# Performance work log

Measured on AMD Instinct MI355X. Metric: run time of the kernel, lower is better.

Reference implementation:

```python
import jax, jax.numpy as jnp
import numpy as np

DIM = 768
HEADS = 12
EXPERTS = 8
HID = 3072  # dim * moe_mlp_ratio(=4)
TOP_K = 2
LN_EPS = 1e-5


def _layer_norm(x, g, b):
    mu = x.mean(-1, keepdims=True)
    var = ((x - mu) ** 2).mean(-1, keepdims=True)
    return (x - mu) * jax.lax.rsqrt(var + LN_EPS) * g + b


def setup_inputs() -> dict:
    key = jax.random.key(0)
    ks = jax.random.split(key, 16)
    s = 0.02
    return {
        "x": jax.random.normal(ks[0], (8, 196, DIM), jnp.float32),
        "ln1_g": jnp.ones((DIM,), jnp.float32),
        "ln1_b": jnp.zeros((DIM,), jnp.float32),
        "qkv_w": jax.random.normal(ks[1], (DIM, 3 * DIM), jnp.float32) * s,
        "qkv_b": jnp.zeros((3 * DIM,), jnp.float32),
        "proj_w": jax.random.normal(ks[2], (DIM, DIM), jnp.float32) * s,
        "proj_b": jnp.zeros((DIM,), jnp.float32),
        "ln2_g": jnp.ones((DIM,), jnp.float32),
        "ln2_b": jnp.zeros((DIM,), jnp.float32),
        "gate_w": jax.random.normal(ks[3], (DIM, EXPERTS), jnp.float32) * s,
        "w1": jax.random.normal(ks[4], (EXPERTS, DIM, HID), jnp.float32) * s,
        "b1": jnp.zeros((EXPERTS, HID), jnp.float32),
        "w2": jax.random.normal(ks[5], (EXPERTS, HID, DIM), jnp.float32) * s,
        "b2": jnp.zeros((EXPERTS, DIM), jnp.float32),
    }


def _attention(x, qkv_w, qkv_b, proj_w, proj_b):
    B, N, C = x.shape
    hd = C // HEADS
    qkv = (x @ qkv_w + qkv_b).reshape(B, N, 3, HEADS, hd).transpose(2, 0, 3, 1, 4)
    q, k, v = qkv[0], qkv[1], qkv[2]  # [B,H,N,hd]
    attn = jax.nn.softmax(jnp.einsum("bhnd,bhmd->bhnm", q, k) * (hd ** -0.5), axis=-1)
    o = jnp.einsum("bhnm,bhmd->bhnd", attn, v).transpose(0, 2, 1, 3).reshape(B, N, C)
    return o @ proj_w + proj_b


def _moe_mlp(xn, gate_w, w1, b1, w2, b2):
    # xn: [T, D]; noisy top-k gate in eval mode (no noise)
    T = xn.shape[0]
    logits = xn @ gate_w                                   # [T, E]
    top_logits, top_idx = jax.lax.top_k(logits, TOP_K)     # [T, k]
    top_gates = jax.nn.softmax(top_logits, axis=-1)        # [T, k]
    gates = jnp.zeros((T, EXPERTS), xn.dtype).at[
        jnp.arange(T)[:, None], top_idx
    ].set(top_gates)                                       # [T, E] sparse combine weights
    # dense-masked expert compute (math identical to dispatch: gate=0 tokens contribute 0)
    h = jax.nn.gelu(jnp.einsum("td,edh->teh", xn, w1) + b1, approximate=False)
    y = jnp.einsum("teh,ehd->ted", h, w2) + b2             # [T, E, D]
    return jnp.einsum("ted,te->td", y, gates)


def reference(x, ln1_g, ln1_b, qkv_w, qkv_b, proj_w, proj_b,
              ln2_g, ln2_b, gate_w, w1, b1, w2, b2):
    B, N, C = x.shape
    x = x + _attention(_layer_norm(x, ln1_g, ln1_b), qkv_w, qkv_b, proj_w, proj_b)
    xn = _layer_norm(x, ln2_g, ln2_b).reshape(B * N, C)
    moe_out = _moe_mlp(xn, gate_w, w1, b1, w2, b2).reshape(B, N, C)
    return x + moe_out
```

## Files before the change

kernel.cpp:

```cpp
#include <hip/hip_runtime.h>
#include <hip/hip_bf16.h>
#include <math.h>

#define DIMC 768
#define HEADS 12
#define HD 64
#define EXPERTS 8
#define HID 3072
#define BB 8
#define NN 196
#define TT (BB*NN)
#define CAP_ROWS 4224
#define LN_EPS 1e-5f

typedef float f32x4_t __attribute__((ext_vector_type(4)));
typedef short bf16x8_t __attribute__((ext_vector_type(8)));
typedef unsigned short u16x8_t __attribute__((ext_vector_type(8)));

__device__ __forceinline__ unsigned short f2bf(float f) {
    unsigned int u = __float_as_uint(f);
    u += 0x7FFFu + ((u >> 16) & 1u);
    return (unsigned short)(u >> 16);
}
__device__ __forceinline__ float bf2f(unsigned short u) {
    return __uint_as_float(((unsigned int)u) << 16);
}

__global__ void ln_kernel(const float* __restrict__ x, const float* __restrict__ g,
                          const float* __restrict__ b, float* __restrict__ out_f,
                          unsigned short* __restrict__ out_hi,
                          unsigned short* __restrict__ out_lo) {
    int t = blockIdx.x;
    const float* xr = x + (size_t)t * DIMC;
    int tid = threadIdx.x;
    float v0 = xr[tid], v1 = xr[tid + 256], v2 = xr[tid + 512];
    __shared__ float red[256];
    red[tid] = v0 + v1 + v2;
    __syncthreads();
    for (int off = 128; off > 0; off >>= 1) {
        if (tid < off) red[tid] += red[tid + off];
        __syncthreads();
    }
    float mu = red[0] * (1.0f / DIMC);
    __syncthreads();
    float d0 = v0 - mu, d1 = v1 - mu, d2 = v2 - mu;
    red[tid] = d0*d0 + d1*d1 + d2*d2;
    __syncthreads();
    for (int off = 128; off > 0; off >>= 1) {
        if (tid < off) red[tid] += red[tid + off];
        __syncthreads();
    }
    float rstd = rsqrtf(red[0] * (1.0f / DIMC) + LN_EPS);
    float o0 = d0 * rstd * g[tid]       + b[tid];
    float o1 = d1 * rstd * g[tid + 256] + b[tid + 256];
    float o2 = d2 * rstd * g[tid + 512] + b[tid + 512];
    if (out_f) {
        float* o = out_f + (size_t)t * DIMC;
        o[tid] = o0; o[tid + 256] = o1; o[tid + 512] = o2;
    }
    if (out_hi) {
        unsigned short* o = out_hi + (size_t)t * DIMC;
        unsigned short h0 = f2bf(o0), h1 = f2bf(o1), h2 = f2bf(o2);
        o[tid] = h0; o[tid + 256] = h1; o[tid + 512] = h2;
        if (out_lo) {
            unsigned short* ol = out_lo + (size_t)t * DIMC;
            ol[tid]       = f2bf(o0 - bf2f(h0));
            ol[tid + 256] = f2bf(o1 - bf2f(h1));
            ol[tid + 512] = f2bf(o2 - bf2f(h2));
        }
    }
}

__global__ void attn_mfma_kernel(const float* __restrict__ qkv,
                                 unsigned short* __restrict__ ao_h,
                                 unsigned short* __restrict__ ao_l) {
    __shared__ float ps[64][224];
    __shared__ unsigned short QsH[64 * 64], QsL[64 * 64];
    __shared__ unsigned short KsH[64 * 64], KsL[64 * 64];

    int bh = blockIdx.x;
    int b = bh / HEADS, h = bh % HEADS;
    int q0 = blockIdx.y * 64;
    const float* base = qkv + (size_t)b * NN * 2304 + h * 64;

    int tid = threadIdx.x;
    int sr = tid >> 3, sq = tid & 7;
    int lane = tid & 63;
    int wid = tid >> 6;
    int wm = (wid >> 1) * 32;
    int wn = (wid & 1) * 32;
    int lrow = lane & 15;
    int lq = lane >> 4;
    int colb_base = lq * 16;

    #pragma unroll
    for (int p = 0; p < 2; ++p) {
        int r = sr + p * 32;
        int n = q0 + r;
        float v[8] = {0.f,0.f,0.f,0.f,0.f,0.f,0.f,0.f};
        if (n < NN) {
            float4 a0 = *(const float4*)(base + (size_t)n * 2304 + sq * 8);
            float4 a1 = *(const float4*)(base + (size_t)n * 2304 + sq * 8 + 4);
            v[0]=a0.x; v[1]=a0.y; v[2]=a0.z; v[3]=a0.w;
            v[4]=a1.x; v[5]=a1.y; v[6]=a1.z; v[7]=a1.w;
        }
        u16x8_t hv, lv;
        #pragma unroll
        for (int t = 0; t < 8; ++t) {
            unsigned short hh = f2bf(v[t]);
            hv[t] = hh; lv[t] = f2bf(v[t] - bf2f(hh));
        }
        int off = r * 128 + ((sq * 16) ^ ((r & 7) << 4));
        *(u16x8_t*)((char*)QsH + off) = hv;
        *(u16x8_t*)((char*)QsL + off) = lv;
    }

    for (int kt = 0; kt < 4; ++kt) {
        int j0 = kt * 64;
        __syncthreads();
        #pragma unroll
        for (int p = 0; p < 2; ++p) {
            int r = sr + p * 32;
            int n = j0 + r;
            float v[8] = {0.f,0.f,0.f,0.f,0.f,0.f,0.f,0.f};
            if (n < NN) {
                float4 a0 = *(const float4*)(base + (size_t)n * 2304 + 768 + sq * 8);
                float4 a1 = *(const float4*)(base + (size_t)n * 2304 + 768 + sq * 8 + 4);
                v[0]=a0.x; v[1]=a0.y; v[2]=a0.z; v[3]=a0.w;
                v[4]=a1.x; v[5]=a1.y; v[6]=a1.z; v[7]=a1.w;
            }
            u16x8_t hv, lv;
            #pragma unroll
            for (int t = 0; t < 8; ++t) {
                unsigned short hh = f2bf(v[t]);
                hv[t] = hh; lv[t] = f2bf(v[t] - bf2f(hh));
            }
            int off = r * 128 + ((sq * 16) ^ ((r & 7) << 4));
            *(u16x8_t*)((char*)KsH + off) = hv;
            *(u16x8_t*)((char*)KsL + off) = lv;
        }
        __syncthreads();

        f32x4_t acc[2][2] = {};
        #pragma unroll
        for (int kk = 0; kk < 2; ++kk) {
            int colb = kk * 64 + colb_base;
            bf16x8_t qh[2], ql[2], kh[2], kl[2];
            #pragma unroll
            for (int i = 0; i < 2; ++i) {
                int ra = wm + i * 16 + lrow;
                int oa = ra * 128 + (colb ^ ((ra & 7) << 4));
                qh[i] = *(const bf16x8_t*)((const char*)QsH + oa);
                ql[i] = *(const bf16x8_t*)((const char*)QsL + oa);
                int rb = wn + i * 16 + lrow;
                int ob = rb * 128 + (colb ^ ((rb & 7) << 4));
                kh[i] = *(const bf16x8_t*)((const char*)KsH + ob);
                kl[i] = *(const bf16x8_t*)((const char*)KsL + ob);
            }
            #pragma unroll
            for (int mi = 0; mi < 2; ++mi)
                #pragma unroll
                for (int ni = 0; ni < 2; ++ni) {
                    acc[mi][ni] = __builtin_amdgcn_mfma_f32_16x16x32_bf16(
                        qh[mi], kh[ni], acc[mi][ni], 0, 0, 0);
                    acc[mi][ni] = __builtin_amdgcn_mfma_f32_16x16x32_bf16(
                        qh[mi], kl[ni], acc[mi][ni], 0, 0, 0);
                    acc[mi][ni] = __builtin_amdgcn_mfma_f32_16x16x32_bf16(
                        ql[mi], kh[ni], acc[mi][ni], 0, 0, 0);
                }
        }
        #pragma unroll
        for (int mi = 0; mi < 2; ++mi)
            #pragma unroll
            for (int ni = 0; ni < 2; ++ni) {
                int jc = j0 + wn + ni * 16 + lrow;
                if (jc < 224) {
                    int rowb = wm + mi * 16 + lq * 4;
                    #pragma unroll
                    for (int j = 0; j < 4; ++j)
                        ps[rowb + j][jc] = acc[mi][ni][j] * 0.125f;
                }
            }
    }
    __syncthreads();

    {
        int i = tid >> 2, l = tid & 3;
        float mx = -1e30f;
        for (int j = l; j < NN; j += 4) mx = fmaxf(mx, ps[i][j]);
        mx = fmaxf(mx, __shfl_xor(mx, 1, 4));
        mx = fmaxf(mx, __shfl_xor(mx, 2, 4));
        float sum = 0.f;
        for (int j = l; j < NN; j += 4) { float e = expf(ps[i][j] - mx); ps[i][j] = e; sum += e; }
        sum += __shfl_xor(sum, 1, 4);
        sum += __shfl_xor(sum, 2, 4);
        float inv = 1.f / sum;
        for (int j = l; j < NN; j += 4) ps[i][j] *= inv;
    }

    f32x4_t oacc[2][2] = {};
    for (int kt = 0; kt < 4; ++kt) {
        int j0 = kt * 64;
        __syncthreads();
        #pragma unroll
        for (int p = 0; p < 2; ++p) {
            int r = sr + p * 32;
            int n = j0 + r;
            float v[8] = {0.f,0.f,0.f,0.f,0.f,0.f,0.f,0.f};
            if (n < NN) {
                float4 a0 = *(const float4*)(base + (size_t)n * 2304 + 1536 + sq * 8);
                float4 a1 = *(const float4*)(base + (size_t)n * 2304 + 1536 + sq * 8 + 4);
                v[0]=a0.x; v[1]=a0.y; v[2]=a0.z; v[3]=a0.w;
                v[4]=a1.x; v[5]=a1.y; v[6]=a1.z; v[7]=a1.w;
            }
            #pragma unroll
            for (int t = 0; t < 8; ++t) {
                int d = sq * 8 + t;
                unsigned short hh = f2bf(v[t]);
                int off = d * 128 + ((r * 2) ^ ((d & 7) << 4));
                *(unsigned short*)((char*)KsH + off) = hh;
                *(unsigned short*)((char*)KsL + off) = f2bf(v[t] - bf2f(hh));
            }
        }
        __syncthreads();

        int kkmax = (kt == 3) ? 1 : 2;
        for (int kk = 0; kk < kkmax; ++kk) {
            int colb = kk * 64 + colb_base;
            bf16x8_t pah[2], pal[2], vh[2], vl[2];
            #pragma unroll
            for (int i = 0; i < 2; ++i) {
                int ra = wm + i * 16 + lrow;
                const float* prow = &ps[ra][j0 + kk * 32 + lq * 8];
                float4 a0 = *(const float4*)prow;
                float4 a1 = *(const float4*)(prow + 4);
                float vv[8] = {a0.x,a0.y,a0.z,a0.w,a1.x,a1.y,a1.z,a1.w};
                u16x8_t hv, lv;
                #pragma unroll
                for (int t = 0; t < 8; ++t) {
                    unsigned short hh = f2bf(vv[t]);
                    hv[t] = hh; lv[t] = f2bf(vv[t] - bf2f(hh));
                }
                pah[i] = *(bf16x8_t*)&hv;
                pal[i] = *(bf16x8_t*)&lv;
                int rb = wn + i * 16 + lrow;
                int ob = rb * 128 + (colb ^ ((rb & 7) << 4));
                vh[i] = *(const bf16x8_t*)((const char*)KsH + ob);
                vl[i] = *(const bf16x8_t*)((const char*)KsL + ob);
            }
            #pragma unroll
            for (int mi = 0; mi < 2; ++mi)
                #pragma unroll
                for (int ni = 0; ni < 2; ++ni) {
                    oacc[mi][ni] = __builtin_amdgcn_mfma_f32_16x16x32_bf16(
                        pah[mi], vh[ni], oacc[mi][ni], 0, 0, 0);
                    oacc[mi][ni] = __builtin_amdgcn_mfma_f32_16x16x32_bf16(
                        pah[mi], vl[ni], oacc[mi][ni], 0, 0, 0);
                    oacc[mi][ni] = __builtin_amdgcn_mfma_f32_16x16x32_bf16(
                        pal[mi], vh[ni], oacc[mi][ni], 0, 0, 0);
                }
        }
    }

    #pragma unroll
    for (int mi = 0; mi < 2; ++mi)
        #pragma unroll
        for (int ni = 0; ni < 2; ++ni) {
            int col = h * 64 + wn + ni * 16 + lrow;
            #pragma unroll
            for (int j = 0; j < 4; ++j) {
                int n = q0 + wm + mi * 16 + lq * 4 + j;
                if (n < NN) {
                    float v = oacc[mi][ni][j];
                    unsigned short hh = f2bf(v);
                    size_t o = (size_t)(b * NN + n) * DIMC + col;
                    ao_h[o] = hh;
                    ao_l[o] = f2bf(v - bf2f(hh));
                }
            }
        }
}

__global__ void gate_kernel(const float* __restrict__ xn, const float* __restrict__ gw,
                            int* __restrict__ tok_e, float* __restrict__ tok_g,
                            int* __restrict__ counts) {
    int t = blockIdx.x;
    int lane = threadIdx.x;
    float acc[8] = {};
    const float* xr = xn + (size_t)t * DIMC;
    for (int i = lane; i < DIMC; i += 64) {
        float xi = xr[i];
        const float* gr = gw + (size_t)i * 8;
        #pragma unroll
        for (int e = 0; e < 8; ++e) acc[e] += xi * gr[e];
    }
    #pragma unroll
    for (int e = 0; e < 8; ++e) {
        #pragma unroll
        for (int off = 32; off > 0; off >>= 1) acc[e] += __shfl_down(acc[e], off, 64);
    }
    if (lane == 0) {
        int e0 = 0; float l0 = acc[0];
        #pragma unroll
        for (int e = 1; e < 8; ++e) if (acc[e] > l0) { l0 = acc[e]; e0 = e; }
        int e1 = -1; float l1 = -3e38f;
        #pragma unroll
        for (int e = 0; e < 8; ++e) if (e != e0 && acc[e] > l1) { l1 = acc[e]; e1 = e; }
        float pp = expf(l1 - l0);
        float g0 = 1.f / (1.f + pp);
        float g1 = pp / (1.f + pp);
        tok_e[t*2] = e0; tok_e[t*2+1] = e1;
        tok_g[t*2] = g0; tok_g[t*2+1] = g1;
        atomicAdd(&counts[e0], 1);
        atomicAdd(&counts[e1], 1);
    }
}

__global__ void init_kernel(int* __restrict__ counts, int* __restrict__ row2tok, int cap) {
    int i = blockIdx.x * blockDim.x + threadIdx.x;
    if (i < 8) counts[i] = 0;
    if (i < cap) row2tok[i] = -1;
}

__global__ void offsets_kernel(const int* __restrict__ counts, int* __restrict__ offsets,
                               int* __restrict__ cursor) {
    if (threadIdx.x == 0 && blockIdx.x == 0) {
        int off = 0;
        for (int e = 0; e < 8; ++e) {
            offsets[e] = off;
            cursor[e]  = off;
            off += ((counts[e] + 63) / 64) * 64;
        }
        offsets[8] = off;
    }
}

__global__ void fill_kernel(const int* __restrict__ tok_e, int* __restrict__ cursor,
                            int* __restrict__ row2tok, int* __restrict__ tok_row) {
    int t = blockIdx.x * blockDim.x + threadIdx.x;
    if (t >= TT) return;
    #pragma unroll
    for (int k = 0; k < 2; ++k) {
        int e = tok_e[t*2+k];
        int slot = atomicAdd(&cursor[e], 1);
        row2tok[slot] = t;
        tok_row[t*2+k] = slot;
    }
}

__global__ void transpose_bf16(const float* __restrict__ src, unsigned short* __restrict__ dst,
                               int R, int C) {
    __shared__ float tile[64][65];
    const float* s = src + (size_t)blockIdx.z * R * C;
    unsigned short* d = dst + (size_t)blockIdx.z * R * C;
    int c0 = blockIdx.x * 64, r0 = blockIdx.y * 64;
    int tid = threadIdx.x;
    int tr = tid >> 4;
    int tc = (tid & 15) * 4;
    #pragma unroll
    for (int p = 0; p < 4; ++p) {
        int r = tr + p * 16;
        const float4 v = *(const float4*)(s + (size_t)(r0 + r) * C + c0 + tc);
        tile[r][tc+0] = v.x; tile[r][tc+1] = v.y; tile[r][tc+2] = v.z; tile[r][tc+3] = v.w;
    }
    __syncthreads();
    #pragma unroll
    for (int p = 0; p < 4; ++p) {
        int c = tr + p * 16;
        ushort4 o;
        o.x = f2bf(tile[tc+0][c]);
        o.y = f2bf(tile[tc+1][c]);
        o.z = f2bf(tile[tc+2][c]);
        o.w = f2bf(tile[tc+3][c]);
        *(ushort4*)(d + (size_t)(c0 + c) * R + r0 + tc) = o;
    }
}

__global__ void transpose_split_bf16(const float* __restrict__ src,
                                     unsigned short* __restrict__ dh,
                                     unsigned short* __restrict__ dl, int R, int C) {
    __shared__ float tile[64][65];
    int c0 = blockIdx.x * 64, r0 = blockIdx.y * 64;
    int tid = threadIdx.x;
    int tr = tid >> 4;
    int tc = (tid & 15) * 4;
    #pragma unroll
    for (int p = 0; p < 4; ++p) {
        int r = tr + p * 16;
        const float4 v = *(const float4*)(src + (size_t)(r0 + r) * C + c0 + tc);
        tile[r][tc+0] = v.x; tile[r][tc+1] = v.y; tile[r][tc+2] = v.z; tile[r][tc+3] = v.w;
    }
    __syncthreads();
    #pragma unroll
    for (int p = 0; p < 4; ++p) {
        int c = tr + p * 16;
        ushort4 h, l;
        float v0 = tile[tc+0][c], v1 = tile[tc+1][c], v2 = tile[tc+2][c], v3 = tile[tc+3][c];
        h.x = f2bf(v0); l.x = f2bf(v0 - bf2f(h.x));
        h.y = f2bf(v1); l.y = f2bf(v1 - bf2f(h.y));
        h.z = f2bf(v2); l.z = f2bf(v2 - bf2f(h.z));
        h.w = f2bf(v3); l.w = f2bf(v3 - bf2f(h.w));
        size_t off = (size_t)(c0 + c) * R + r0 + tc;
        *(ushort4*)(dh + off) = h;
        *(ushort4*)(dl + off) = l;
    }
}

template<int RES>
__global__ void mfma_gemm_split(const unsigned short* __restrict__ Ah,
                                const unsigned short* __restrict__ Al,
                                const unsigned short* __restrict__ Bth,
                                const unsigned short* __restrict__ Btl,
                                const float* __restrict__ bias,
                                const float* __restrict__ res,
                                float* __restrict__ C,
                                int M, int N, int K) {
    __shared__ unsigned short AsH[64 * 64];
    __shared__ unsigned short AsL[64 * 64];
    __shared__ unsigned short BsH[64 * 64];
    __shared__ unsigned short BsL[64 * 64];

    int m0 = blockIdx.x * 64;
    int n0 = blockIdx.y * 64;
    int tid = threadIdx.x;
    int sr = tid >> 3;
    int sq = tid & 7;
    int lane = tid & 63;
    int wid = tid >> 6;
    int wm = (wid >> 1) * 32;
    int wn = (wid & 1) * 32;
    int colb_base = (lane >> 4) * 16;
    int lrow = lane & 15;

    f32x4_t acc[2][2] = {};

    for (int k0 = 0; k0 < K; k0 += 64) {
        #pragma unroll
        for (int p = 0; p < 2; ++p) {
            int r = sr + p * 32;
            int swz = (sq * 16) ^ ((r & 7) << 4);
            int4 vah = {0,0,0,0}, val = {0,0,0,0};
            if (m0 + r < M) {
                size_t aoff = (size_t)(m0 + r) * K + k0 + sq * 8;
                vah = *(const int4*)(Ah + aoff);
                val = *(const int4*)(Al + aoff);
            }
            *(int4*)((char*)AsH + r * 128 + swz) = vah;
            *(int4*)((char*)AsL + r * 128 + swz) = val;
            size_t boff = (size_t)(n0 + r) * K + k0 + sq * 8;
            *(int4*)((char*)BsH + r * 128 + swz) = *(const int4*)(Bth + boff);
            *(int4*)((char*)BsL + r * 128 + swz) = *(const int4*)(Btl + boff);
        }
        __syncthreads();
        #pragma unroll
        for (int kk = 0; kk < 2; ++kk) {
            int colb = kk * 64 + colb_base;
            bf16x8_t ah[2], al[2], bh[2], bl[2];
            #pragma unroll
            for (int i = 0; i < 2; ++i) {
                int ra = wm + i * 16 + lrow;
                int oa = ra * 128 + (colb ^ ((ra & 7) << 4));
                ah[i] = *(const bf16x8_t*)((const char*)AsH + oa);
                al[i] = *(const bf16x8_t*)((const char*)AsL + oa);
                int rb = wn + i * 16 + lrow;
                int ob = rb * 128 + (colb ^ ((rb & 7) << 4));
                bh[i] = *(const bf16x8_t*)((const char*)BsH + ob);
                bl[i] = *(const bf16x8_t*)((const char*)BsL + ob);
            }
            #pragma unroll
            for (int mi = 0; mi < 2; ++mi)
                #pragma unroll
                for (int ni = 0; ni < 2; ++ni) {
                    acc[mi][ni] = __builtin_amdgcn_mfma_f32_16x16x32_bf16(
                        ah[mi], bh[ni], acc[mi][ni], 0, 0, 0);
                    acc[mi][ni] = __builtin_amdgcn_mfma_f32_16x16x32_bf16(
                        ah[mi], bl[ni], acc[mi][ni], 0, 0, 0);
                    acc[mi][ni] = __builtin_amdgcn_mfma_f32_16x16x32_bf16(
                        al[mi], bh[ni], acc[mi][ni], 0, 0, 0);
                }
        }
        __syncthreads();
    }

    #pragma unroll
    for (int mi = 0; mi < 2; ++mi) {
        #pragma unroll
        for (int ni = 0; ni < 2; ++ni) {
            int col = n0 + wn + ni * 16 + lrow;
            #pragma unroll
            for (int j = 0; j < 4; ++j) {
                int row = m0 + wm + mi * 16 + (lane >> 4) * 4 + j;
                if (row < M) {
                    float v = acc[mi][ni][j] + bias[col];
                    if (RES) v += res[(size_t)row * N + col];
                    C[(size_t)row * N + col] = v;
                }
            }
        }
    }
}

template<int GATHER, int GELU, int OUT_BF16>
__global__ void mfma_gemm_grouped(const unsigned short* __restrict__ A,
                                  const unsigned short* __restrict__ Bt,
                                  const float* __restrict__ bias,
                                  const int* __restrict__ offsets,
                                  const int* __restrict__ row2tok,
                                  void* __restrict__ Cout,
                                  int N, int K, int nxb) {
    __shared__ unsigned short As[64 * 64];
    __shared__ unsigned short Bs[64 * 64];
    __shared__ int toks[64];

    int nwg = gridDim.x;
    int pbid = blockIdx.x;
    int q = nwg >> 3, r8 = nwg & 7;
    int xcd = pbid & 7, slot = pbid >> 3;
    int L = (xcd < r8) ? xcd * (q + 1) + slot
                       : r8 * (q + 1) + (xcd - r8) * q + slot;
    int xb = L % nxb;
    int n0 = (L / nxb) * 64;
    int r0 = xb * 64;
    if (r0 >= offsets[8]) return;
    int e = 0;
    while (r0 >= offsets[e + 1]) ++e;

    int tid = threadIdx.x;
    if (GATHER && tid < 64) toks[tid] = row2tok[r0 + tid];
    __syncthreads();

    const unsigned short* Be = Bt + (size_t)e * N * K;

    int sr = tid >> 3;
    int sq = tid & 7;
    int lane = tid & 63;
    int wid = tid >> 6;
    int wm = (wid >> 1) * 32;
    int wn = (wid & 1) * 32;
    int colb_base = (lane >> 4) * 16;
    int lrow = lane & 15;

    f32x4_t acc[2][2] = {};

    for (int k0 = 0; k0 < K; k0 += 64) {
        #pragma unroll
        for (int p = 0; p < 2; ++p) {
            int r = sr + p * 32;
            int swz = (sq * 16) ^ ((r & 7) << 4);
            int4 va = {0, 0, 0, 0};
            if (GATHER) {
                int tok = toks[r];
                if (tok >= 0) va = *(const int4*)(A + (size_t)tok * K + k0 + sq * 8);
            } else {
                va = *(const int4*)(A + (size_t)(r0 + r) * K + k0 + sq * 8);
            }
            *(int4*)((char*)As + r * 128 + swz) = va;
            int4 vb = *(const int4*)(Be + (size_t)(n0 + r) * K + k0 + sq * 8);
            *(int4*)((char*)Bs + r * 128 + swz) = vb;
        }
        __syncthreads();
        #pragma unroll
        for (int kk = 0; kk < 2; ++kk) {
            int colb = kk * 64 + colb_base;
            bf16x8_t a[2], b[2];
            #pragma unroll
            for (int i = 0; i < 2; ++i) {
                int ra = wm + i * 16 + lrow;
                a[i] = *(const bf16x8_t*)((const char*)As + ra * 128 + (colb ^ ((ra & 7) << 4)));
                int rb = wn + i * 16 + lrow;
                b[i] = *(const bf16x8_t*)((const char*)Bs + rb * 128 + (colb ^ ((rb & 7) << 4)));
            }
            #pragma unroll
            for (int mi = 0; mi < 2; ++mi)
                #pragma unroll
                for (int ni = 0; ni < 2; ++ni)
                    acc[mi][ni] = __builtin_amdgcn_mfma_f32_16x16x32_bf16(
                        a[mi], b[ni], acc[mi][ni], 0, 0, 0);
        }
        __syncthreads();
    }

    #pragma unroll
    for (int mi = 0; mi < 2; ++mi) {
        #pragma unroll
        for (int ni = 0; ni < 2; ++ni) {
            int col = n0 + wn + ni * 16 + lrow;
            float bv = GELU ? bias[(size_t)e * N + col] : 0.f;
            #pragma unroll
            for (int j = 0; j < 4; ++j) {
                int row = r0 + wm + mi * 16 + (lane >> 4) * 4 + j;
                float v = acc[mi][ni][j] + bv;
                if (GELU) v = 0.5f * v * (1.f + erff(v * 0.70710678f));
                if (OUT_BF16)
                    ((unsigned short*)Cout)[(size_t)row * N + col] = f2bf(v);
                else
                    ((float*)Cout)[(size_t)row * N + col] = v;
            }
        }
    }
}

__global__ void combine_kernel(const float* __restrict__ x_res, const float* __restrict__ y,
                               const float* __restrict__ b2, const int* __restrict__ tok_e,
                               const float* __restrict__ tok_g, const int* __restrict__ tok_row,
                               float* __restrict__ out) {
    int t = blockIdx.x;
    int c = blockIdx.y * 256 + threadIdx.x;
    int e0 = tok_e[t*2], e1 = tok_e[t*2+1];
    float g0 = tok_g[t*2], g1 = tok_g[t*2+1];
    int r0 = tok_row[t*2], r1 = tok_row[t*2+1];
    float v = x_res[(size_t)t * DIMC + c]
            + g0 * (y[(size_t)r0 * DIMC + c] + b2[(size_t)e0 * DIMC + c])
            + g1 * (y[(size_t)r1 * DIMC + c] + b2[(size_t)e1 * DIMC + c]);
    out[(size_t)t * DIMC + c] = v;
}

extern "C" void kernel_launch(void* const* d_in, const int* in_sizes, int n_in,
                              void* d_out, int out_size, void* d_ws, size_t ws_size,
                              hipStream_t stream) {
    const float* x      = (const float*)d_in[0];
    const float* ln1_g  = (const float*)d_in[1];
    const float* ln1_b  = (const float*)d_in[2];
    const float* qkv_w  = (const float*)d_in[3];
    const float* qkv_b  = (const float*)d_in[4];
    const float* proj_w = (const float*)d_in[5];
    const float* proj_b = (const float*)d_in[6];
    const float* ln2_g  = (const float*)d_in[7];
    const float* ln2_b  = (const float*)d_in[8];
    const float* gate_w = (const float*)d_in[9];
    const float* w1     = (const float*)d_in[10];
    const float* b1     = (const float*)d_in[11];
    const float* w2     = (const float*)d_in[12];
    const float* b2     = (const float*)d_in[13];
    float* out = (float*)d_out;

    char* p = (char*)d_ws;
    auto alloc = [&](size_t nbytes) {
        void* r = (void*)p;
        p += (nbytes + 255) & ~(size_t)255;
        return r;
    };
    unsigned short* xn1_h   = (unsigned short*)alloc((size_t)TT * DIMC * 2);
    unsigned short* xn1_l   = (unsigned short*)alloc((size_t)TT * DIMC * 2);
    float*          qkv     = (float*)alloc((size_t)TT * 2304 * 4);
    unsigned short* ao_h    = (unsigned short*)alloc((size_t)TT * DIMC * 2);
    unsigned short* ao_l    = (unsigned short*)alloc((size_t)TT * DIMC * 2);
    float*          x_res   = (float*)alloc((size_t)TT * DIMC * 4);
    float*          xn2_f   = (float*)alloc((size_t)TT * DIMC * 4);
    unsigned short* xn2_bf  = (unsigned short*)alloc((size_t)TT * DIMC * 2);
    unsigned short* h       = (unsigned short*)alloc((size_t)CAP_ROWS * HID * 2);
    float*          y       = (float*)alloc((size_t)CAP_ROWS * DIMC * 4);
    unsigned short* w1t     = (unsigned short*)alloc((size_t)EXPERTS * DIMC * HID * 2);
    unsigned short* w2t     = (unsigned short*)alloc((size_t)EXPERTS * DIMC * HID * 2);
    unsigned short* qwt_h   = (unsigned short*)alloc((size_t)DIMC * 2304 * 2);
    unsigned short* qwt_l   = (unsigned short*)alloc((size_t)DIMC * 2304 * 2);
    unsigned short* pwt_h   = (unsigned short*)alloc((size_t)DIMC * DIMC * 2);
    unsigned short* pwt_l   = (unsigned short*)alloc((size_t)DIMC * DIMC * 2);
    float*          tok_g   = (float*)alloc((size_t)2 * TT * 4);
    int*            tok_e   = (int*)alloc((size_t)2 * TT * 4);
    int*            tok_row = (int*)alloc((size_t)2 * TT * 4);
    int*            row2tok = (int*)alloc((size_t)CAP_ROWS * 4);
    int*            counts  = (int*)alloc(32 * 4);
    int*            offsets = (int*)alloc(32 * 4);
    int*            cursor  = (int*)alloc(32 * 4);

    init_kernel<<<(CAP_ROWS + 255) / 256, 256, 0, stream>>>(counts, row2tok, CAP_ROWS);

    transpose_bf16<<<dim3(HID / 64, DIMC / 64, EXPERTS), 256, 0, stream>>>(w1, w1t, DIMC, HID);
    transpose_bf16<<<dim3(DIMC / 64, HID / 64, EXPERTS), 256, 0, stream>>>(w2, w2t, HID, DIMC);
    transpose_split_bf16<<<dim3(2304 / 64, DIMC / 64), 256, 0, stream>>>(qkv_w, qwt_h, qwt_l,
                                                                         DIMC, 2304);
    transpose_split_bf16<<<dim3(DIMC / 64, DIMC / 64), 256, 0, stream>>>(proj_w, pwt_h, pwt_l,
                                                                         DIMC, DIMC);

    ln_kernel<<<TT, 256, 0, stream>>>(x, ln1_g, ln1_b, nullptr, xn1_h, xn1_l);

    mfma_gemm_split<0><<<dim3((TT + 63) / 64, 2304 / 64), 256, 0, stream>>>(
        xn1_h, xn1_l, qwt_h, qwt_l, qkv_b, nullptr, qkv, TT, 2304, DIMC);

    attn_mfma_kernel<<<dim3(BB * HEADS, 4), 256, 0, stream>>>(qkv, ao_h, ao_l);

    mfma_gemm_split<1><<<dim3((TT + 63) / 64, DIMC / 64), 256, 0, stream>>>(
        ao_h, ao_l, pwt_h, pwt_l, proj_b, x, x_res, TT, DIMC, DIMC);

    ln_kernel<<<TT, 256, 0, stream>>>(x_res, ln2_g, ln2_b, xn2_f, xn2_bf, nullptr);

    gate_kernel<<<TT, 64, 0, stream>>>(xn2_f, gate_w, tok_e, tok_g, counts);

    offsets_kernel<<<1, 64, 0, stream>>>(counts, offsets, cursor);

    fill_kernel<<<(TT + 255) / 256, 256, 0, stream>>>(tok_e, cursor, row2tok, tok_row);

    {
        int nxb = CAP_ROWS / 64;
        int nwg1 = (HID / 64) * nxb;
        mfma_gemm_grouped<1, 1, 1><<<nwg1, 256, 0, stream>>>(
            xn2_bf, w1t, b1, offsets, row2tok, h, HID, DIMC, nxb);

        int nwg2 = (DIMC / 64) * nxb;
        mfma_gemm_grouped<0, 0, 0><<<nwg2, 256, 0, stream>>>(
            h, w2t, nullptr, offsets, row2tok, y, DIMC, HID, nxb);
    }

    combine_kernel<<<dim3(TT, 3), 256, 0, stream>>>(x_res, y, b2, tok_e, tok_g, tok_row, out);
}
```

Measured before the change: 309.5 us.

## Double attention block threads to 512 and swizzle score buffer in LDS

The attention kernel now runs 8 waves per block instead of 4. Each wave handles a 32x16 output tile, so it does half the MFMA work of the old 32x32 tile, and the staging loops load one row per thread instead of two. The score matrix is stored in a flat byte buffer with an XOR swizzle, and the V tile swizzle is extended, to reduce LDS bank conflicts. Softmax now uses 8 threads per row. This adds latency hiding and parallelism to a kernel that only launches 384 blocks, at the cost of more redundant Q fragment loads per wave.

```diff
diff --git a/kernel.cpp b/kernel.cpp
--- a/kernel.cpp
+++ b/kernel.cpp
@@ -74,7 +74,7 @@
 __global__ void attn_mfma_kernel(const float* __restrict__ qkv,
                                  unsigned short* __restrict__ ao_h,
                                  unsigned short* __restrict__ ao_l) {
-    __shared__ float ps[64][224];
+    __shared__ char psb[64 * 896];
     __shared__ unsigned short QsH[64 * 64], QsL[64 * 64];
     __shared__ unsigned short KsH[64 * 64], KsL[64 * 64];
 
@@ -87,15 +87,14 @@
     int sr = tid >> 3, sq = tid & 7;
     int lane = tid & 63;
     int wid = tid >> 6;
-    int wm = (wid >> 1) * 32;
-    int wn = (wid & 1) * 32;
+    int wm = (wid >> 2) * 32;
+    int wn = (wid & 3) * 16;
     int lrow = lane & 15;
     int lq = lane >> 4;
     int colb_base = lq * 16;
 
-    #pragma unroll
-    for (int p = 0; p < 2; ++p) {
-        int r = sr + p * 32;
+    {
+        int r = sr;
         int n = q0 + r;
         float v[8] = {0.f,0.f,0.f,0.f,0.f,0.f,0.f,0.f};
         if (n < NN) {
@@ -118,9 +117,8 @@
     for (int kt = 0; kt < 4; ++kt) {
         int j0 = kt * 64;
         __syncthreads();
-        #pragma unroll
-        for (int p = 0; p < 2; ++p) {
-            int r = sr + p * 32;
+        {
+            int r = sr;
             int n = j0 + r;
             float v[8] = {0.f,0.f,0.f,0.f,0.f,0.f,0.f,0.f};
             if (n < NN) {
@@ -141,70 +139,74 @@
         }
         __syncthreads();
 
-        f32x4_t acc[2][2] = {};
+        f32x4_t acc[2] = {};
         #pragma unroll
         for (int kk = 0; kk < 2; ++kk) {
             int colb = kk * 64 + colb_base;
-            bf16x8_t qh[2], ql[2], kh[2], kl[2];
+            bf16x8_t qh[2], ql[2], kh, kl;
             #pragma unroll
             for (int i = 0; i < 2; ++i) {
                 int ra = wm + i * 16 + lrow;
                 int oa = ra * 128 + (colb ^ ((ra & 7) << 4));
                 qh[i] = *(const bf16x8_t*)((const char*)QsH + oa);
                 ql[i] = *(const bf16x8_t*)((const char*)QsL + oa);
-                int rb = wn + i * 16 + lrow;
-                int ob = rb * 128 + (colb ^ ((rb & 7) << 4));
-                kh[i] = *(const bf16x8_t*)((const char*)KsH + ob);
-                kl[i] = *(const bf16x8_t*)((const char*)KsL + ob);
-            }
-            #pragma unroll
-            for (int mi = 0; mi < 2; ++mi)
+            }
+            int rb = wn + lrow;
+            int ob = rb * 128 + (colb ^ ((rb & 7) << 4));
+            kh = *(const bf16x8_t*)((const char*)KsH + ob);
+            kl = *(const bf16x8_t*)((const char*)KsL + ob);
+            #pragma unroll
+            for (int mi = 0; mi < 2; ++mi) {
+                acc[mi] = __builtin_amdgcn_mfma_f32_16x16x32_bf16(qh[mi], kh, acc[mi], 0, 0, 0);
+                acc[mi] = __builtin_amdgcn_mfma_f32_16x16x32_bf16(qh[mi], kl, acc[mi], 0, 0, 0);
+                acc[mi] = __builtin_amdgcn_mfma_f32_16x16x32_bf16(ql[mi], kh, acc[mi], 0, 0, 0);
+            }
+        }
+        int jc = j0 + wn + lrow;
+        if (jc < 224) {
+            #pragma unroll
+            for (int mi = 0; mi < 2; ++mi) {
                 #pragma unroll
-                for (int ni = 0; ni < 2; ++ni) {
-                    acc[mi][ni] = __builtin_amdgcn_mfma_f32_16x16x32_bf16(
-                        qh[mi], kh[ni], acc[mi][ni], 0, 0, 0);
-                    acc[mi][ni] = __builtin_amdgcn_mfma_f32_16x16x32_bf16(
-                        qh[mi], kl[ni], acc[mi][ni], 0, 0, 0);
-                    acc[mi][ni] = __builtin_amdgcn_mfma_f32_16x16x32_bf16(
-                        ql[mi], kh[ni], acc[mi][ni], 0, 0, 0);
+                for (int j = 0; j < 4; ++j) {
+                    int row = wm + mi * 16 + lq * 4 + j;
+                    int s = (row & 7) ^ (row >> 3);
+                    *(float*)(psb + row * 896 + ((jc * 4) ^ (s << 4))) = acc[mi][j] * 0.125f;
                 }
-        }
-        #pragma unroll
-        for (int mi = 0; mi < 2; ++mi)
-            #pragma unroll
-            for (int ni = 0; ni < 2; ++ni) {
-                int jc = j0 + wn + ni * 16 + lrow;
-                if (jc < 224) {
-                    int rowb = wm + mi * 16 + lq * 4;
-                    #pragma unroll
-                    for (int j = 0; j < 4; ++j)
-                        ps[rowb + j][jc] = acc[mi][ni][j] * 0.125f;
-                }
-            }
+            }
+        }
     }
     __syncthreads();
 
     {
-        int i = tid >> 2, l = tid & 3;
+        int i = tid >> 3, l = tid & 7;
+        int s = (i & 7) ^ (i >> 3);
+        char* prow = psb + i * 896;
         float mx = -1e30f;
-        for (int j = l; j < NN; j += 4) mx = fmaxf(mx, ps[i][j]);
-        mx = fmaxf(mx, __shfl_xor(mx, 1, 4));
-        mx = fmaxf(mx, __shfl_xor(mx, 2, 4));
+        for (int j = l; j < NN; j += 8) mx = fmaxf(mx, *(const float*)(prow + ((j * 4) ^ (s << 4))));
+        mx = fmaxf(mx, __shfl_xor(mx, 1, 8));
+        mx = fmaxf(mx, __shfl_xor(mx, 2, 8));
+        mx = fmaxf(mx, __shfl_xor(mx, 4, 8));
         float sum = 0.f;
-        for (int j = l; j < NN; j += 4) { float e = expf(ps[i][j] - mx); ps[i][j] = e; sum += e; }
-        sum += __shfl_xor(sum, 1, 4);
-        sum += __shfl_xor(sum, 2, 4);
+        for (int j = l; j < NN; j += 8) {
+            float* pp = (float*)(prow + ((j * 4) ^ (s << 4)));
+            float e = expf(*pp - mx); *pp = e; sum += e;
+        }
+        sum += __shfl_xor(sum, 1, 8);
+        sum += __shfl_xor(sum, 2, 8);
+        sum += __shfl_xor(sum, 4, 8);
         float inv = 1.f / sum;
-        for (int j = l; j < NN; j += 4) ps[i][j] *= inv;
-    }
-
-    f32x4_t oacc[2][2] = {};
+        for (int j = l; j < NN; j += 8) {
+            float* pp = (float*)(prow + ((j * 4) ^ (s << 4)));
+            *pp *= inv;
+        }
+    }
+
+    f32x4_t oacc[2] = {};
     for (int kt = 0; kt < 4; ++kt) {
         int j0 = kt * 64;
         __syncthreads();
-        #pragma unroll
-        for (int p = 0; p < 2; ++p) {
-            int r = sr + p * 32;
+        {
+            int r = sr;
             int n = j0 + r;
             float v[8] = {0.f,0.f,0.f,0.f,0.f,0.f,0.f,0.f};
             if (n < NN) {
@@ -216,8 +218,9 @@
             #pragma unroll
             for (int t = 0; t < 8; ++t) {
                 int d = sq * 8 + t;
+                int sw = ((d & 7) ^ (d >> 3)) << 4;
                 unsigned short hh = f2bf(v[t]);
-                int off = d * 128 + ((r * 2) ^ ((d & 7) << 4));
+                int off = d * 128 + ((r * 2) ^ sw);
                 *(unsigned short*)((char*)KsH + off) = hh;
                 *(unsigned short*)((char*)KsL + off) = f2bf(v[t] - bf2f(hh));
             }
@@ -227,13 +230,15 @@
         int kkmax = (kt == 3) ? 1 : 2;
         for (int kk = 0; kk < kkmax; ++kk) {
             int colb = kk * 64 + colb_base;
-            bf16x8_t pah[2], pal[2], vh[2], vl[2];
+            bf16x8_t pah[2], pal[2], vh, vl;
             #pragma unroll
             for (int i = 0; i < 2; ++i) {
                 int ra = wm + i * 16 + lrow;
-                const float* prow = &ps[ra][j0 + kk * 32 + lq * 8];
-                float4 a0 = *(const float4*)prow;
-                float4 a1 = *(const float4*)(prow + 4);
+                int s = (ra & 7) ^ (ra >> 3);
+                const char* prow = psb + ra * 896;
+                int jb = (j0 + kk * 32 + lq * 8) * 4;
+                float4 a0 = *(const float4*)(prow + (jb ^ (s << 4)));
+                float4 a1 = *(const float4*)(prow + ((jb + 16) ^ (s << 4)));
                 float vv[8] = {a0.x,a0.y,a0.z,a0.w,a1.x,a1.y,a1.z,a1.w};
                 u16x8_t hv, lv;
                 #pragma unroll
@@ -243,42 +248,35 @@
                 }
                 pah[i] = *(bf16x8_t*)&hv;
                 pal[i] = *(bf16x8_t*)&lv;
-                int rb = wn + i * 16 + lrow;
-                int ob = rb * 128 + (colb ^ ((rb & 7) << 4));
-                vh[i] = *(const bf16x8_t*)((const char*)KsH + ob);
-                vl[i] = *(const bf16x8_t*)((const char*)KsL + ob);
-            }
-            #pragma unroll
-            for (int mi = 0; mi < 2; ++mi)
-                #pragma unroll
-                for (int ni = 0; ni < 2; ++ni) {
-                    oacc[mi][ni] = __builtin_amdgcn_mfma_f32_16x16x32_bf16(
-                        pah[mi], vh[ni], oacc[mi][ni], 0, 0, 0);
-                    oacc[mi][ni] = __builtin_amdgcn_mfma_f32_16x16x32_bf16(
-                        pah[mi], vl[ni], oacc[mi][ni], 0, 0, 0);
-                    oacc[mi][ni] = __builtin_amdgcn_mfma_f32_16x16x32_bf16(
-                        pal[mi], vh[ni], oacc[mi][ni], 0, 0, 0);
-                }
-        }
-    }
-
-    #pragma unroll
-    for (int mi = 0; mi < 2; ++mi)
-        #pragma unroll
-        for (int ni = 0; ni < 2; ++ni) {
-            int col = h * 64 + wn + ni * 16 + lrow;
-            #pragma unroll
-            for (int j = 0; j < 4; ++j) {
-                int n = q0 + wm + mi * 16 + lq * 4 + j;
-                if (n < NN) {
-                    float v = oacc[mi][ni][j];
-                    unsigned short hh = f2bf(v);
-                    size_t o = (size_t)(b * NN + n) * DIMC + col;
-                    ao_h[o] = hh;
-                    ao_l[o] = f2bf(v - bf2f(hh));
-                }
-            }
-        }
+            }
+            int rb = wn + lrow;
+            int ob = rb * 128 + (colb ^ (((rb & 7) ^ (rb >> 3)) << 4));
+            vh = *(const bf16x8_t*)((const char*)KsH + ob);
+            vl = *(const bf16x8_t*)((const char*)KsL + ob);
+            #pragma unroll
+            for (int mi = 0; mi < 2; ++mi) {
+                oacc[mi] = __builtin_amdgcn_mfma_f32_16x16x32_bf16(pah[mi], vh, oacc[mi], 0, 0, 0);
+                oacc[mi] = __builtin_amdgcn_mfma_f32_16x16x32_bf16(pah[mi], vl, oacc[mi], 0, 0, 0);
+                oacc[mi] = __builtin_amdgcn_mfma_f32_16x16x32_bf16(pal[mi], vh, oacc[mi], 0, 0, 0);
+            }
+        }
+    }
+
+    #pragma unroll
+    for (int mi = 0; mi < 2; ++mi) {
+        int col = h * 64 + wn + lrow;
+        #pragma unroll
+        for (int j = 0; j < 4; ++j) {
+            int n = q0 + wm + mi * 16 + lq * 4 + j;
+            if (n < NN) {
+                float v = oacc[mi][j];
+                unsigned short hh = f2bf(v);
+                size_t o = (size_t)(b * NN + n) * DIMC + col;
+                ao_h[o] = hh;
+                ao_l[o] = f2bf(v - bf2f(hh));
+            }
+        }
+    }
 }
 
 __global__ void gate_kernel(const float* __restrict__ xn, const float* __restrict__ gw,
@@ -678,7 +676,7 @@
     mfma_gemm_split<0><<<dim3((TT + 63) / 64, 2304 / 64), 256, 0, stream>>>(
         xn1_h, xn1_l, qwt_h, qwt_l, qkv_b, nullptr, qkv, TT, 2304, DIMC);
 
-    attn_mfma_kernel<<<dim3(BB * HEADS, 4), 256, 0, stream>>>(qkv, ao_h, ao_l);
+    attn_mfma_kernel<<<dim3(BB * HEADS, 4), 512, 0, stream>>>(qkv, ao_h, ao_l);
 
     mfma_gemm_split<1><<<dim3((TT + 63) / 64, DIMC / 64), 256, 0, stream>>>(
         ao_h, ao_l, pwt_h, pwt_l, proj_b, x, x_res, TT, DIMC, DIMC);
```

Measured after the change: 296.3 us. -4.3%, faster.
